# Kernel optimization log

Measured on AMD Instinct MI355X. Metric: run time of the kernel, lower is better.

Reference implementation:

```python
import jax, jax.numpy as jnp
import numpy as np

B, C_IN, T, IMG, P = 4, 3, 8, 224, 16
E, DEPTH, D_INNER, N_ST, DT_R, K = 384, 24, 768, 16, 24, 4
HP = IMG // P
NP_ = HP * HP          # 196 patches per frame
L = T * NP_            # 1568 tokens
EPS = 1e-5


def setup_inputs():
    key = jax.random.key(0)
    ks = jax.random.split(key, 24)
    r = lambda k, s, sc=0.02: jax.random.normal(k, s, jnp.float32) * sc
    inp = {
        "x": jax.random.normal(ks[0], (B, C_IN, T, IMG, IMG), jnp.float32),
        "patch_w": r(ks[1], (E, C_IN, 1, P, P)),
        "patch_b": jnp.zeros((E,), jnp.float32),
        "pos_embed": r(ks[2], (NP_, E)),
        "temporal_pos": r(ks[3], (T, E)),
        "imp_w1": r(ks[4], (E, E)),
        "imp_b1": jnp.zeros((E,), jnp.float32),
        "imp_w2": r(ks[5], (1, E)),
        "imp_b2": jnp.zeros((1,), jnp.float32),
        "in_w": r(ks[6], (DEPTH, 2 * D_INNER, E)),
        "out_w": r(ks[7], (DEPTH, E, D_INNER)),
        "norm_w": jnp.ones((DEPTH, E), jnp.float32),
        "norm_f_w": jnp.ones((E,), jnp.float32),
    }
    A_row = jnp.log(jnp.arange(1, N_ST + 1, dtype=jnp.float32))  # S4D-real init
    for i, sfx in enumerate(["", "_b"]):
        b = 8 + 4 * i
        inp["conv_w" + sfx] = r(ks[b], (DEPTH, D_INNER, K), 0.1)
        inp["conv_b" + sfx] = jnp.zeros((DEPTH, D_INNER), jnp.float32)
        inp["xp_w" + sfx] = r(ks[b + 1], (DEPTH, DT_R + 2 * N_ST, D_INNER))
        inp["dt_w" + sfx] = r(ks[b + 2], (DEPTH, D_INNER, DT_R), 0.01)
        inp["dt_b" + sfx] = jax.random.uniform(ks[b + 3], (DEPTH, D_INNER), jnp.float32, -4.6, -2.3)
        inp["A_log" + sfx] = jnp.tile(A_row, (DEPTH, D_INNER, 1))
        inp["D" + sfx] = jnp.ones((DEPTH, D_INNER), jnp.float32)
    return inp


def rmsnorm(x, w):
    x = x.astype(jnp.float32)
    return x * jax.lax.rsqrt(jnp.mean(x * x, axis=-1, keepdims=True) + EPS) * w


def causal_conv1d(x, w, b):
    # x: [B,L,D]; depthwise causal conv with kernel K
    xt = x.transpose(0, 2, 1)  # B D L
    y = jax.lax.conv_general_dilated(
        xt, w[:, None, :], (1,), [(K - 1, 0)],
        dimension_numbers=("NCH", "OIH", "NCH"), feature_group_count=D_INNER)
    return (y + b[None, :, None]).transpose(0, 2, 1)


def selective_scan(xt, dt, Bm, Cm, A, Dp):
    # xt,dt: [B,L,D]; Bm,Cm: [B,L,N]; A: [D,N]
    def step(h, ins):
        dt_t, x_t, B_t, C_t = ins  # [B,D],[B,D],[B,N],[B,N]
        h = h * jnp.exp(dt_t[..., None] * A) + (dt_t * x_t)[..., None] * B_t[:, None, :]
        return h, jnp.einsum('bdn,bn->bd', h, C_t)
    h0 = jnp.zeros((xt.shape[0], D_INNER, N_ST), xt.dtype)
    xs = (dt.transpose(1, 0, 2), xt.transpose(1, 0, 2),
          Bm.transpose(1, 0, 2), Cm.transpose(1, 0, 2))
    _, ys = jax.lax.scan(step, h0, xs)
    return ys.transpose(1, 0, 2) + xt * Dp


def mamba_dir(xc, z, cw, cb, xpw, dtw, dtb, Alog, Dp):
    xt = jax.nn.silu(causal_conv1d(xc, cw, cb))
    dbc = jnp.einsum('bld,ed->ble', xt, xpw)
    dt_low = dbc[..., :DT_R]
    Bm = dbc[..., DT_R:DT_R + N_ST]
    Cm = dbc[..., DT_R + N_ST:]
    dt = jax.nn.softplus(jnp.einsum('blr,dr->bld', dt_low, dtw) + dtb)
    y = selective_scan(xt, dt, Bm, Cm, -jnp.exp(Alog), Dp)
    return y * jax.nn.silu(z)


def mamba_block(h, p):
    xz = jnp.einsum('ble,fe->blf', h, p['in_w'])
    xc, z = xz[..., :D_INNER], xz[..., D_INNER:]
    yf = mamba_dir(xc, z, p['conv_w'], p['conv_b'], p['xp_w'], p['dt_w'], p['dt_b'], p['A_log'], p['D'])
    flip = lambda t: t[:, ::-1, :]
    yb = flip(mamba_dir(flip(xc), flip(z), p['conv_w_b'], p['conv_b_b'], p['xp_w_b'],
                        p['dt_w_b'], p['dt_b_b'], p['A_log_b'], p['D_b']))
    return jnp.einsum('bld,ed->ble', yf + yb, p['out_w'])


def _encoder(x, patch_w, patch_b, pos_embed, temporal_pos, imp_w1, imp_b1, imp_w2, imp_b2,
             in_w, out_w, norm_w, norm_f_w,
             conv_w, conv_b, xp_w, dt_w, dt_b, A_log, D,
             conv_w_b, conv_b_b, xp_w_b, dt_w_b, dt_b_b, A_log_b, D_b, mixer=mamba_block):
    Bn = x.shape[0]
    # PatchEmbed: Conv3d kernel (1,P,P) stride (1,P,P) == patchify + matmul
    xp = x.reshape(Bn, C_IN, T, HP, P, HP, P)
    xp = xp.transpose(0, 2, 3, 5, 1, 4, 6).reshape(Bn, T, NP_, C_IN * P * P)
    tok = xp @ patch_w.reshape(E, C_IN * P * P).T + patch_b  # [B,T,N,E]
    tok = tok + pos_embed[None, None] + temporal_pos[None, :, None, :]
    xseq = tok.reshape(Bn, L, E)
    # token importance gating
    h1 = jax.nn.relu(xseq @ imp_w1.T + imp_b1)
    logits = (h1 @ imp_w2.T + imp_b2)[..., 0]  # [B,L]
    xseq = xseq * jax.nn.sigmoid(logits)[..., None]
    stacked = {'in_w': in_w, 'out_w': out_w, 'norm_w': norm_w,
               'conv_w': conv_w, 'conv_b': conv_b, 'xp_w': xp_w, 'dt_w': dt_w,
               'dt_b': dt_b, 'A_log': A_log, 'D': D,
               'conv_w_b': conv_w_b, 'conv_b_b': conv_b_b, 'xp_w_b': xp_w_b,
               'dt_w_b': dt_w_b, 'dt_b_b': dt_b_b, 'A_log_b': A_log_b, 'D_b': D_b}

    def layer_fn(carry, p):
        hidden, residual = carry
        residual = (hidden + residual).astype(jnp.float32)  # fused add-norm, prenorm
        hn = rmsnorm(residual, p['norm_w'])
        hidden = mixer(hn, p)
        return (hidden, residual), None

    (hidden, residual), _ = jax.lax.scan(layer_fn, (xseq, jnp.zeros_like(xseq)), stacked)
    feats = rmsnorm(hidden + residual, norm_f_w)
    return feats, logits


def reference(x, patch_w, patch_b, pos_embed, temporal_pos, imp_w1, imp_b1, imp_w2, imp_b2,
              in_w, out_w, norm_w, norm_f_w,
              conv_w, conv_b, xp_w, dt_w, dt_b, A_log, D,
              conv_w_b, conv_b_b, xp_w_b, dt_w_b, dt_b_b, A_log_b, D_b):
    return _encoder(x, patch_w, patch_b, pos_embed, temporal_pos, imp_w1, imp_b1, imp_w2, imp_b2,
                    in_w, out_w, norm_w, norm_f_w,
                    conv_w, conv_b, xp_w, dt_w, dt_b, A_log, D,
                    conv_w_b, conv_b_b, xp_w_b, dt_w_b, dt_b_b, A_log_b, D_b)
```

## Files before the change

### kernel.cpp

```cpp
#include <hip/hip_runtime.h>
#include <hip/hip_bf16.h>

#define LL 1568
#define EE 384
#define DD 768
#define BB 4

typedef float f32x4 __attribute__((ext_vector_type(4)));
typedef float f32x2 __attribute__((ext_vector_type(2)));
typedef unsigned short u16x2 __attribute__((ext_vector_type(2)));
typedef unsigned short u16x4 __attribute__((ext_vector_type(4)));
typedef unsigned short u16x8 __attribute__((ext_vector_type(8)));
typedef __bf16 bf16x8 __attribute__((ext_vector_type(8)));

__device__ inline unsigned short f2bf(float f) {
    unsigned int u = __builtin_bit_cast(unsigned int, f);
    u += 0x7fffu + ((u >> 16) & 1u);
    return (unsigned short)(u >> 16);
}
__device__ inline float bf2f(unsigned short u) {
    unsigned int v = ((unsigned int)u) << 16;
    return __builtin_bit_cast(float, v);
}
__device__ inline float silu_f(float v) { return v / (1.f + __expf(-v)); }
__device__ inline float exp2_f(float v) { return __builtin_amdgcn_exp2f(v); }

__global__ __launch_bounds__(256) void k_cvt(const float* __restrict__ src,
                                             unsigned short* __restrict__ dst, int n4) {
    int i = blockIdx.x * 256 + threadIdx.x;
    int stride = gridDim.x * 256;
    for (; i < n4; i += stride) {
        f32x4 v = *(const f32x4*)(src + (size_t)i * 4);
        u16x4 o;
#pragma unroll
        for (int j = 0; j < 4; j++) o[j] = f2bf(v[j]);
        *(u16x4*)(dst + (size_t)i * 4) = o;
    }
}

__global__ __launch_bounds__(256) void k_pad_xpw(const float* __restrict__ src,
                                                 unsigned short* __restrict__ dst) {
    const int total = 24 * 64 * 768;
    for (int i = blockIdx.x * 256 + threadIdx.x; i < total; i += gridDim.x * 256) {
        int l = i / (64 * 768);
        int r = (i / 768) % 64;
        int dcol = i % 768;
        dst[i] = (r < 56) ? f2bf(src[((size_t)l * 56 + r) * 768 + dcol]) : (unsigned short)0;
    }
}

__global__ __launch_bounds__(256) void k_pad_dtw(const float* __restrict__ src,
                                                 unsigned short* __restrict__ dst) {
    const int total = 24 * 768 * 32;
    for (int i = blockIdx.x * 256 + threadIdx.x; i < total; i += gridDim.x * 256) {
        int kk = i & 31;
        int nrow = i >> 5;
        dst[i] = (kk < 24) ? f2bf(src[(size_t)nrow * 24 + kk]) : (unsigned short)0;
    }
}

__global__ __launch_bounds__(256) void k_patch(const float* __restrict__ x,
                                               unsigned short* __restrict__ patches) {
    int bid = blockIdx.x;
    int b = bid / LL, rr = bid % LL, t = rr / 196, pp = rr % 196, hp = pp / 14, wp = pp % 14;
    for (int k = threadIdx.x; k < 768; k += 256) {
        int c = k >> 8, rem = k & 255, i = rem >> 4, j = rem & 15;
        patches[(size_t)bid * 768 + k] =
            f2bf(x[(((size_t)(b * 3 + c) * 8 + t) * 224 + hp * 16 + i) * 224 + wp * 16 + j]);
    }
}

template <int EPI, bool ASUM, bool OUTBF>
__global__ __launch_bounds__(256) void k_gemm(
    const unsigned short* __restrict__ A, const unsigned short* __restrict__ A2,
    const unsigned short* __restrict__ W,
    float* __restrict__ C, unsigned short* __restrict__ Cb, int K, int ldc,
    const float* __restrict__ bias,
    const float* __restrict__ pos, const float* __restrict__ tpos) {
    const int tid = threadIdx.x;
    const int m0 = blockIdx.y * 128;
    const int n0 = blockIdx.x * 128;
    __shared__ unsigned short As[128 * 40];
    __shared__ unsigned short Ws[128 * 40];
    const int sr = tid >> 2;
    const int skc = tid & 3;

    f32x4 acc[4][4];
#pragma unroll
    for (int mi = 0; mi < 4; mi++)
#pragma unroll
        for (int ni = 0; ni < 4; ni++) acc[mi][ni] = (f32x4){0.f, 0.f, 0.f, 0.f};

    const int lane = tid & 63;
    const int wv = tid >> 6;
    const int wm = (wv & 1) << 6;
    const int wn = (wv >> 1) << 6;
    const int lr = lane & 15;
    const int kg = lane >> 4;

    u16x8 ar[2], wr_[2];
    auto loadT = [&](int kt) {
#pragma unroll
        for (int i = 0; i < 2; i++) {
            size_t ka = (size_t)(m0 + sr + 64 * i) * K + kt * 32 + skc * 8;
            u16x8 v = *(const u16x8*)(A + ka);
            if constexpr (ASUM) {
                u16x8 v2 = *(const u16x8*)(A2 + ka);
#pragma unroll
                for (int j = 0; j < 8; j++) v[j] = f2bf(bf2f(v[j]) + bf2f(v2[j]));
            }
            ar[i] = v;
            wr_[i] = *(const u16x8*)(W + (size_t)(n0 + sr + 64 * i) * K + kt * 32 + skc * 8);
        }
    };

    const int nK = K >> 5;
    loadT(0);
    for (int kt = 0; kt < nK; ++kt) {
#pragma unroll
        for (int i = 0; i < 2; i++) {
            *(u16x8*)&As[(sr + 64 * i) * 40 + skc * 8] = ar[i];
            *(u16x8*)&Ws[(sr + 64 * i) * 40 + skc * 8] = wr_[i];
        }
        __syncthreads();
        if (kt + 1 < nK) loadT(kt + 1);
        bf16x8 af[4], bfm[4];
#pragma unroll
        for (int mi = 0; mi < 4; mi++)
            af[mi] = *(const bf16x8*)&As[(wm + mi * 16 + lr) * 40 + kg * 8];
#pragma unroll
        for (int ni = 0; ni < 4; ni++)
            bfm[ni] = *(const bf16x8*)&Ws[(wn + ni * 16 + lr) * 40 + kg * 8];
#pragma unroll
        for (int mi = 0; mi < 4; mi++)
#pragma unroll
            for (int ni = 0; ni < 4; ni++)
                acc[mi][ni] = __builtin_amdgcn_mfma_f32_16x16x32_bf16(af[mi], bfm[ni], acc[mi][ni], 0, 0, 0);
        __syncthreads();
    }

#pragma unroll
    for (int mi = 0; mi < 4; mi++)
#pragma unroll
        for (int ni = 0; ni < 4; ni++)
#pragma unroll
            for (int j = 0; j < 4; j++) {
                int m = m0 + wm + mi * 16 + kg * 4 + j;
                int n = n0 + wn + ni * 16 + lr;
                float v = acc[mi][ni][j];
                if constexpr (EPI == 1) {
                    int rr = m % LL;
                    int t = rr / 196, p = rr % 196;
                    v += bias[n] + pos[p * EE + n] + tpos[t * EE + n];
                    C[(size_t)m * ldc + n] = v;
                    Cb[(size_t)m * ldc + n] = f2bf(v);
                } else if constexpr (EPI == 2) {
                    v += bias[n];
                    v = fmaxf(v, 0.f);
                    C[(size_t)m * ldc + n] = v;
                } else {
                    if constexpr (OUTBF)
                        Cb[(size_t)m * ldc + n] = f2bf(v);
                    else
                        C[(size_t)m * ldc + n] = v;
                }
            }
}

__global__ __launch_bounds__(64) void k_logits(const float* __restrict__ h1, const float* __restrict__ w2,
                                               const float* __restrict__ b2, float* __restrict__ xseq,
                                               float* __restrict__ logits_out) {
    int row = blockIdx.x;
    int lane = threadIdx.x;
    float acc = 0.f;
#pragma unroll
    for (int i = 0; i < 6; i++) {
        int e = lane + i * 64;
        acc += h1[(size_t)row * EE + e] * w2[e];
    }
#pragma unroll
    for (int off = 32; off >= 1; off >>= 1) acc += __shfl_xor(acc, off);
    float logit = acc + b2[0];
    if (lane == 0) logits_out[row] = logit;
    float sg = 1.f / (1.f + __expf(-logit));
#pragma unroll
    for (int i = 0; i < 6; i++) {
        int e = lane + i * 64;
        xseq[(size_t)row * EE + e] *= sg;
    }
}

template <bool OBF>
__global__ __launch_bounds__(256) void k_norm(const float* __restrict__ hidden, float* __restrict__ resid,
                                              const float* __restrict__ wn, float* __restrict__ outf,
                                              unsigned short* __restrict__ outb,
                                              int first, int writeResid) {
    int row = blockIdx.x * 4 + (threadIdx.x >> 6);
    int lane = threadIdx.x & 63;
    size_t base = (size_t)row * EE;
    float v[6];
    float ss = 0.f;
#pragma unroll
    for (int i = 0; i < 6; i++) {
        int e = lane + i * 64;
        float h = hidden[base + e];
        float r = first ? 0.f : resid[base + e];
        float s = h + r;
        v[i] = s;
        ss += s * s;
    }
#pragma unroll
    for (int off = 32; off >= 1; off >>= 1) ss += __shfl_xor(ss, off);
    if (writeResid) {
#pragma unroll
        for (int i = 0; i < 6; i++) resid[base + lane + i * 64] = v[i];
    }
    float sc = rsqrtf(ss * (1.f / 384.f) + 1e-5f);
#pragma unroll
    for (int i = 0; i < 6; i++) {
        int e = lane + i * 64;
        float o = v[i] * sc * wn[e];
        if constexpr (OBF)
            outb[base + e] = f2bf(o);
        else
            outf[base + e] = o;
    }
}

__global__ __launch_bounds__(256) void k_conv(
    const unsigned short* __restrict__ xz,
    const float* __restrict__ cw_f, const float* __restrict__ cb_f,
    const float* __restrict__ cw_b, const float* __restrict__ cb_b,
    unsigned short* __restrict__ xtb) {
    const int tid = threadIdx.x;
    if (tid >= 192) return;
    const int b = blockIdx.y, dir = blockIdx.z;
    const float* cw = dir ? cw_b : cw_f;
    const float* cb = dir ? cb_b : cb_f;
    const int o = tid % 96, tg = tid / 96;
    const int t0 = blockIdx.x * 16 + tg * 8;
    const int d0 = o * 8;
    const size_t xzb = (size_t)b * LL * 1536;
    const size_t obase = ((size_t)dir * BB + b) * LL;

    f32x4 wq[8];
    float bv[8];
#pragma unroll
    for (int j = 0; j < 8; j++) {
        wq[j] = *(const f32x4*)&cw[(d0 + j) * 4];
        bv[j] = cb[d0 + j];
    }

    auto loadrow = [&](int t) -> u16x8 {
        if (t < 0) return (u16x8){0, 0, 0, 0, 0, 0, 0, 0};
        int phys = dir ? (LL - 1 - t) : t;
        return *(const u16x8*)&xz[xzb + (size_t)phys * 1536 + d0];
    };

    float f0[8], f1[8], f2[8];
    u16x8 v;
    v = loadrow(t0 - 3);
#pragma unroll
    for (int j = 0; j < 8; j++) f0[j] = bf2f(v[j]);
    v = loadrow(t0 - 2);
#pragma unroll
    for (int j = 0; j < 8; j++) f1[j] = bf2f(v[j]);
    v = loadrow(t0 - 1);
#pragma unroll
    for (int j = 0; j < 8; j++) f2[j] = bf2f(v[j]);

    for (int s = 0; s < 8; ++s) {
        int t = t0 + s;
        v = loadrow(t);
        float f3[8];
        u16x8 outv;
#pragma unroll
        for (int j = 0; j < 8; j++) {
            f3[j] = bf2f(v[j]);
            float cv = wq[j][0] * f0[j] + wq[j][1] * f1[j] + wq[j][2] * f2[j] + wq[j][3] * f3[j] + bv[j];
            outv[j] = f2bf(silu_f(cv));
        }
        *(u16x8*)&xtb[(obase + t) * 768 + d0] = outv;
#pragma unroll
        for (int j = 0; j < 8; j++) { f0[j] = f1[j]; f1[j] = f2[j]; f2[j] = f3[j]; }
    }
}

__global__ __launch_bounds__(256) void k_dbc(
    const unsigned short* __restrict__ xtb,
    const unsigned short* __restrict__ xpwb_f, const unsigned short* __restrict__ xpwb_b,
    const unsigned short* __restrict__ dtwb_f, const unsigned short* __restrict__ dtwb_b,
    const float* __restrict__ dtb_f, const float* __restrict__ dtb_b,
    unsigned short* __restrict__ g_dt, float* __restrict__ Bm, float* __restrict__ Cm) {
    const int tid = threadIdx.x;
    const int m0 = blockIdx.x * 64;
    const bool bwd = (m0 >= 6272);
    const unsigned short* W = bwd ? xpwb_b : xpwb_f;
    __shared__ unsigned short As[64 * 40];
    __shared__ unsigned short Ws[64 * 40];
    __shared__ unsigned short Ds[64 * 40];
    const int sr = tid >> 2, skc = tid & 3;
    const int lane = tid & 63, wv = tid >> 6;
    const int lr = lane & 15, kg = lane >> 4;

    f32x4 acc[4];
#pragma unroll
    for (int mi = 0; mi < 4; mi++) acc[mi] = (f32x4){0.f, 0.f, 0.f, 0.f};

    u16x8 ar, wr_;
    auto loadT = [&](int kt) {
        ar = *(const u16x8*)(xtb + (size_t)(m0 + sr) * 768 + kt * 32 + skc * 8);
        wr_ = *(const u16x8*)(W + (size_t)sr * 768 + kt * 32 + skc * 8);
    };
    loadT(0);
    for (int kt = 0; kt < 24; ++kt) {
        *(u16x8*)&As[sr * 40 + skc * 8] = ar;
        *(u16x8*)&Ws[sr * 40 + skc * 8] = wr_;
        __syncthreads();
        if (kt + 1 < 24) loadT(kt + 1);
        bf16x8 bfm = *(const bf16x8*)&Ws[(wv * 16 + lr) * 40 + kg * 8];
#pragma unroll
        for (int mi = 0; mi < 4; mi++) {
            bf16x8 af = *(const bf16x8*)&As[(mi * 16 + lr) * 40 + kg * 8];
            acc[mi] = __builtin_amdgcn_mfma_f32_16x16x32_bf16(af, bfm, acc[mi], 0, 0, 0);
        }
        __syncthreads();
    }
#pragma unroll
    for (int mi = 0; mi < 4; mi++)
#pragma unroll
        for (int j = 0; j < 4; j++) {
            int r = mi * 16 + kg * 4 + j;
            int row = m0 + r;
            int cc = wv * 16 + lr;
            float vv = acc[mi][j];
            if (cc < 32) Ds[r * 40 + cc] = (cc < 24) ? f2bf(vv) : (unsigned short)0;
            if (cc >= 24 && cc < 40) Bm[(size_t)row * 16 + (cc - 24)] = vv;
            else if (cc >= 40 && cc < 56) Cm[(size_t)row * 16 + (cc - 40)] = vv;
        }
    __syncthreads();

    const unsigned short* dtw = bwd ? dtwb_b : dtwb_f;
    const float* dbias = bwd ? dtb_b : dtb_f;
    bf16x8 af2[4];
#pragma unroll
    for (int mi = 0; mi < 4; mi++)
        af2[mi] = *(const bf16x8*)&Ds[(mi * 16 + lr) * 40 + kg * 8];
    for (int nt = wv; nt < 12; nt += 4) {
        int n0 = nt * 64;
        f32x4 acc2[4][4];
#pragma unroll
        for (int mi = 0; mi < 4; mi++)
#pragma unroll
            for (int ni = 0; ni < 4; ni++) acc2[mi][ni] = (f32x4){0.f, 0.f, 0.f, 0.f};
        bf16x8 bfr[4];
#pragma unroll
        for (int ni = 0; ni < 4; ni++)
            bfr[ni] = *(const bf16x8*)(dtw + (size_t)(n0 + ni * 16 + lr) * 32 + kg * 8);
#pragma unroll
        for (int mi = 0; mi < 4; mi++)
#pragma unroll
            for (int ni = 0; ni < 4; ni++)
                acc2[mi][ni] = __builtin_amdgcn_mfma_f32_16x16x32_bf16(af2[mi], bfr[ni], acc2[mi][ni], 0, 0, 0);
#pragma unroll
        for (int mi = 0; mi < 4; mi++)
#pragma unroll
            for (int ni = 0; ni < 4; ni++)
#pragma unroll
                for (int j = 0; j < 4; j++) {
                    int r = mi * 16 + kg * 4 + j;
                    int n = n0 + ni * 16 + lr;
                    float v = acc2[mi][ni][j] + dbias[n];
                    float sp = (v > 20.f) ? v : log1pf(__expf(v));
                    g_dt[(size_t)(m0 + r) * 768 + n] = f2bf(sp);
                }
    }
}

__global__ __launch_bounds__(512) void k_scan(
    const unsigned short* __restrict__ xtb, const unsigned short* __restrict__ dtb,
    const unsigned short* __restrict__ xz,
    const float* __restrict__ Bmat, const float* __restrict__ Cmat,
    const float* __restrict__ Alog_f, const float* __restrict__ Alog_b,
    const float* __restrict__ Dp_f, const float* __restrict__ Dp_b,
    unsigned short* __restrict__ ybuf) {
    const int tid = threadIdx.x;
    const int dl = tid & 15, c = tid >> 4;
    const int d0 = blockIdx.x * 32 + dl * 2;
    const int b = blockIdx.y, dir = blockIdx.z;
    const float* Alog = dir ? Alog_b : Alog_f;
    const float* Dp = dir ? Dp_b : Dp_f;
    const int t0 = c * 49;

    __shared__ float Ssh[32][32][17];
    __shared__ float sdt_sh[32][32];

    float anA[16], anB[16];
#pragma unroll
    for (int n = 0; n < 16; n++) {
        anA[n] = -__expf(Alog[d0 * 16 + n]) * 1.44269504f;
        anB[n] = -__expf(Alog[(d0 + 1) * 16 + n]) * 1.44269504f;
    }
    bool unif = (anA[0] != 0.f) && (anB[0] != 0.f);
#pragma unroll
    for (int n = 1; n < 16; n++) {
        float rA = anA[n] / anA[0];
        float rB = anB[n] / anB[0];
        unif = unif && (fabsf(rA - (float)(n + 1)) < 1e-3f) && (fabsf(rB - (float)(n + 1)) < 1e-3f);
    }
    const float a0A = anA[0], a0B = anB[0];
    float DdA = Dp[d0], DdB = Dp[d0 + 1];

    const size_t dbase = ((size_t)dir * BB + b) * LL;
    const size_t rowb = dbase * 768 + d0;

    f32x2 SA[8], SB[8];
#pragma unroll
    for (int k = 0; k < 8; k++) { SA[k] = (f32x2){0.f, 0.f}; SB[k] = (f32x2){0.f, 0.f}; }
    float sumA = 0.f, sumB = 0.f;

    for (int s = 0; s < 49; ++s) {
        int t = t0 + s;
        unsigned int xv = *(const unsigned int*)&xtb[rowb + (size_t)t * 768];
        unsigned int dv = *(const unsigned int*)&dtb[rowb + (size_t)t * 768];
        float xtA = bf2f((unsigned short)xv), xtB = bf2f((unsigned short)(xv >> 16));
        float dtA = bf2f((unsigned short)dv), dtB = bf2f((unsigned short)(dv >> 16));
        sumA += dtA; sumB += dtB;
        float dxA = dtA * xtA, dxB = dtB * xtB;
        const f32x4* Bp = (const f32x4*)(Bmat + (dbase + t) * 16);
        f32x4 Bq[4] = {Bp[0], Bp[1], Bp[2], Bp[3]};
        const f32x2* B2 = (const f32x2*)Bq;
        f32x2 dxA2 = {dxA, dxA}, dxB2 = {dxB, dxB};
        if (unif) {
            float pA = exp2_f(dtA * a0A), pB = exp2_f(dtB * a0B);
            float qA = pA * pA, qB = pB * pB;
            f32x2 qA2 = {qA, qA}, qB2 = {qB, qB};
            f32x2 pwA[8], pwB[8];
            pwA[0] = (f32x2){pA, qA};
            pwB[0] = (f32x2){pB, qB};
#pragma unroll
            for (int j = 1; j < 8; j++) { pwA[j] = pwA[j - 1] * qA2; pwB[j] = pwB[j - 1] * qB2; }
#pragma unroll
            for (int k = 0; k < 8; k++) {
                SA[k] = SA[k] * pwA[k] + dxA2 * B2[k];
                SB[k] = SB[k] * pwB[k] + dxB2 * B2[k];
            }
        } else {
#pragma unroll
            for (int n = 0; n < 16; n++) {
                float bqv = ((const float*)Bq)[n];
                float eA = exp2_f(dtA * anA[n]);
                float eB = exp2_f(dtB * anB[n]);
                SA[n >> 1][n & 1] = SA[n >> 1][n & 1] * eA + dxA * bqv;
                SB[n >> 1][n & 1] = SB[n >> 1][n & 1] * eB + dxB * bqv;
            }
        }
    }
#pragma unroll
    for (int n = 0; n < 16; n++) {
        Ssh[c][dl * 2][n] = SA[n >> 1][n & 1];
        Ssh[c][dl * 2 + 1][n] = SB[n >> 1][n & 1];
    }
    sdt_sh[c][dl * 2] = sumA;
    sdt_sh[c][dl * 2 + 1] = sumB;
    __syncthreads();

    {
        int cdl = tid & 31, n2 = tid >> 5;
        float a_n = -__expf(Alog[(blockIdx.x * 32 + cdl) * 16 + n2]) * 1.44269504f;
        float H = 0.f;
#pragma unroll
        for (int c2 = 0; c2 < 32; c2++) {
            float P = exp2_f(a_n * sdt_sh[c2][cdl]);
            float tmp = Ssh[c2][cdl][n2];
            Ssh[c2][cdl][n2] = H;
            H = H * P + tmp;
        }
    }
    __syncthreads();

#pragma unroll
    for (int n = 0; n < 16; n++) {
        SA[n >> 1][n & 1] = Ssh[c][dl * 2][n];
        SB[n >> 1][n & 1] = Ssh[c][dl * 2 + 1][n];
    }
    for (int s = 0; s < 49; ++s) {
        int t = t0 + s;
        unsigned int xv = *(const unsigned int*)&xtb[rowb + (size_t)t * 768];
        unsigned int dv = *(const unsigned int*)&dtb[rowb + (size_t)t * 768];
        float xtA = bf2f((unsigned short)xv), xtB = bf2f((unsigned short)(xv >> 16));
        float dtA = bf2f((unsigned short)dv), dtB = bf2f((unsigned short)(dv >> 16));
        float dxA = dtA * xtA, dxB = dtB * xtB;
        const f32x4* Bp = (const f32x4*)(Bmat + (dbase + t) * 16);
        f32x4 Bq[4] = {Bp[0], Bp[1], Bp[2], Bp[3]};
        const f32x4* Cp = (const f32x4*)(Cmat + (dbase + t) * 16);
        f32x4 Cq[4] = {Cp[0], Cp[1], Cp[2], Cp[3]};
        const f32x2* B2 = (const f32x2*)Bq;
        const f32x2* C2 = (const f32x2*)Cq;
        f32x2 dxA2 = {dxA, dxA}, dxB2 = {dxB, dxB};
        f32x2 yA2 = {0.f, 0.f}, yB2 = {0.f, 0.f};
        if (unif) {
            float pA = exp2_f(dtA * a0A), pB = exp2_f(dtB * a0B);
            float qA = pA * pA, qB = pB * pB;
            f32x2 qA2 = {qA, qA}, qB2 = {qB, qB};
            f32x2 pwA[8], pwB[8];
            pwA[0] = (f32x2){pA, qA};
            pwB[0] = (f32x2){pB, qB};
#pragma unroll
            for (int j = 1; j < 8; j++) { pwA[j] = pwA[j - 1] * qA2; pwB[j] = pwB[j - 1] * qB2; }
#pragma unroll
            for (int k = 0; k < 8; k++) {
                SA[k] = SA[k] * pwA[k] + dxA2 * B2[k];
                SB[k] = SB[k] * pwB[k] + dxB2 * B2[k];
                yA2 = yA2 + SA[k] * C2[k];
                yB2 = yB2 + SB[k] * C2[k];
            }
        } else {
#pragma unroll
            for (int n = 0; n < 16; n++) {
                float bqv = ((const float*)Bq)[n];
                float cqv = ((const float*)Cq)[n];
                float eA = exp2_f(dtA * anA[n]);
                float eB = exp2_f(dtB * anB[n]);
                float sA = SA[n >> 1][n & 1] * eA + dxA * bqv;
                float sB = SB[n >> 1][n & 1] * eB + dxB * bqv;
                SA[n >> 1][n & 1] = sA;
                SB[n >> 1][n & 1] = sB;
                yA2[n & 1] += sA * cqv;
                yB2[n & 1] += sB * cqv;
            }
        }
        float yA = yA2[0] + yA2[1] + xtA * DdA;
        float yB = yB2[0] + yB2[1] + xtB * DdB;
        int pt = dir ? (LL - 1 - t) : t;
        unsigned int zv2 = *(const unsigned int*)&xz[((size_t)b * LL + pt) * 1536 + 768 + d0];
        float zA = bf2f((unsigned short)zv2), zB = bf2f((unsigned short)(zv2 >> 16));
        unsigned int yo = (unsigned int)f2bf(yA * silu_f(zA)) |
                          ((unsigned int)f2bf(yB * silu_f(zB)) << 16);
        *(unsigned int*)&ybuf[rowb + (size_t)pt * 768] = yo;
    }
}

extern "C" void kernel_launch(void* const* d_in, const int* in_sizes, int n_in,
                              void* d_out, int out_size, void* d_ws, size_t ws_size,
                              hipStream_t stream) {
    const float* x        = (const float*)d_in[0];
    const float* patch_w  = (const float*)d_in[1];
    const float* patch_b  = (const float*)d_in[2];
    const float* pos_emb  = (const float*)d_in[3];
    const float* tpos     = (const float*)d_in[4];
    const float* imp_w1   = (const float*)d_in[5];
    const float* imp_b1   = (const float*)d_in[6];
    const float* imp_w2   = (const float*)d_in[7];
    const float* imp_b2   = (const float*)d_in[8];
    const float* in_w     = (const float*)d_in[9];
    const float* out_w    = (const float*)d_in[10];
    const float* norm_w   = (const float*)d_in[11];
    const float* norm_f_w = (const float*)d_in[12];
    const float* conv_w   = (const float*)d_in[13];
    const float* conv_b   = (const float*)d_in[14];
    const float* xp_w     = (const float*)d_in[15];
    const float* dt_w     = (const float*)d_in[16];
    const float* dt_b     = (const float*)d_in[17];
    const float* A_log    = (const float*)d_in[18];
    const float* Dp       = (const float*)d_in[19];
    const float* conv_w_b = (const float*)d_in[20];
    const float* conv_b_b = (const float*)d_in[21];
    const float* xp_w_b   = (const float*)d_in[22];
    const float* dt_w_b   = (const float*)d_in[23];
    const float* dt_b_b   = (const float*)d_in[24];
    const float* A_log_b  = (const float*)d_in[25];
    const float* D_b      = (const float*)d_in[26];

    float* out = (float*)d_out;
    float* logits_out = out + 2408448;

    char* wsb = (char*)d_ws;
    size_t off = 0;
    auto carve = [&](size_t bytes) { char* p = wsb + off; off += bytes; return p; };

    unsigned short* in_wb    = (unsigned short*)carve(28311552);
    unsigned short* out_wb   = (unsigned short*)carve(14155776);
    unsigned short* patch_wb = (unsigned short*)carve(589824);
    unsigned short* imp_w1b  = (unsigned short*)carve(294912);
    unsigned short* xpwb_f   = (unsigned short*)carve(2359296);
    unsigned short* xpwb_b   = (unsigned short*)carve(2359296);
    unsigned short* dtwb_f   = (unsigned short*)carve(1179648);
    unsigned short* dtwb_b   = (unsigned short*)carve(1179648);
    float*          hidden   = (float*)carve(9633792);
    float*          resid    = (float*)carve(9633792);
    unsigned short* hn       = (unsigned short*)carve(4816896);
    unsigned short* xzb      = (unsigned short*)carve(19267584);
    unsigned short* xtb      = (unsigned short*)carve(19267584);
    unsigned short* g_dt     = (unsigned short*)carve(19267584);
    float*          Bm       = (float*)carve(802816);
    float*          Cm       = (float*)carve(802816);
    unsigned short* ybuf     = (unsigned short*)carve(19267584);

    float*          h1       = (float*)xtb;
    unsigned short* hidb     = (unsigned short*)g_dt;
    unsigned short* patches  = (unsigned short*)ybuf;

    k_cvt<<<2048, 256, 0, stream>>>(in_w, in_wb, 3538944);
    k_cvt<<<2048, 256, 0, stream>>>(out_w, out_wb, 1769472);
    k_cvt<<<288, 256, 0, stream>>>(patch_w, patch_wb, 73728);
    k_cvt<<<144, 256, 0, stream>>>(imp_w1, imp_w1b, 36864);
    k_pad_xpw<<<1024, 256, 0, stream>>>(xp_w, xpwb_f);
    k_pad_xpw<<<1024, 256, 0, stream>>>(xp_w_b, xpwb_b);
    k_pad_dtw<<<1024, 256, 0, stream>>>(dt_w, dtwb_f);
    k_pad_dtw<<<1024, 256, 0, stream>>>(dt_w_b, dtwb_b);

    k_patch<<<6272, 256, 0, stream>>>(x, patches);
    k_gemm<1, false, false><<<dim3(3, 49), 256, 0, stream>>>(patches, nullptr, patch_wb,
                                                             hidden, hidb, 768, 384,
                                                             patch_b, pos_emb, tpos);
    k_gemm<2, false, false><<<dim3(3, 49), 256, 0, stream>>>(hidb, nullptr, imp_w1b,
                                                             h1, nullptr, 384, 384,
                                                             imp_b1, nullptr, nullptr);
    k_logits<<<6272, 64, 0, stream>>>(h1, imp_w2, imp_b2, hidden, logits_out);

    for (int l = 0; l < 24; ++l) {
        k_norm<true><<<1568, 256, 0, stream>>>(hidden, resid, norm_w + l * 384, nullptr, hn,
                                               (l == 0) ? 1 : 0, 1);
        k_gemm<0, false, true><<<dim3(12, 49), 256, 0, stream>>>(hn, nullptr,
                                                                 in_wb + (size_t)l * 589824,
                                                                 nullptr, xzb, 384, 1536,
                                                                 nullptr, nullptr, nullptr);
        k_conv<<<dim3(98, 4, 2), 256, 0, stream>>>(xzb, conv_w + l * 3072, conv_b + l * 768,
                                                   conv_w_b + l * 3072, conv_b_b + l * 768, xtb);
        k_dbc<<<196, 256, 0, stream>>>(xtb, xpwb_f + (size_t)l * 49152, xpwb_b + (size_t)l * 49152,
                                       dtwb_f + (size_t)l * 24576, dtwb_b + (size_t)l * 24576,
                                       dt_b + l * 768, dt_b_b + l * 768,
                                       g_dt, Bm, Cm);
        k_scan<<<dim3(24, 4, 2), 512, 0, stream>>>(
            xtb, g_dt, xzb, Bm, Cm,
            A_log + l * 12288, A_log_b + l * 12288,
            Dp + l * 768, D_b + l * 768,
            ybuf);
        k_gemm<0, true, false><<<dim3(3, 49), 256, 0, stream>>>(ybuf, ybuf + 4816896,
                                                                out_wb + (size_t)l * 294912,
                                                                hidden, nullptr, 768, 384,
                                                                nullptr, nullptr, nullptr);
    }
    k_norm<false><<<1568, 256, 0, stream>>>(hidden, resid, norm_f_w, out, nullptr, 0, 0);
}
```

Baseline: 5.280 ms.

## Split dt projection out of k_dbc into a separate tiled GEMM launch

The fused k_dbc kernel previously did both the x-projection and the dt up-projection (K=32 to 768 with softplus) inside only 196 blocks. The change has k_dbc write a padded 32-wide low-rank dt buffer to global memory, then launches the generic GEMM with a new softplus epilogue over a 6x98 grid. The epilogue picks forward or backward weights and bias by row. This spreads the dt GEMM and the expensive softplus across many more blocks, at the cost of an extra launch and a small global round-trip per layer.

```diff
diff --git a/kernel.cpp b/kernel.cpp
--- a/kernel.cpp
+++ b/kernel.cpp
@@ -73,9 +73,9 @@
 template <int EPI, bool ASUM, bool OUTBF>
 __global__ __launch_bounds__(256) void k_gemm(
     const unsigned short* __restrict__ A, const unsigned short* __restrict__ A2,
-    const unsigned short* __restrict__ W,
+    const unsigned short* __restrict__ W, const unsigned short* __restrict__ W2,
     float* __restrict__ C, unsigned short* __restrict__ Cb, int K, int ldc,
-    const float* __restrict__ bias,
+    const float* __restrict__ bias, const float* __restrict__ bias2,
     const float* __restrict__ pos, const float* __restrict__ tpos) {
     const int tid = threadIdx.x;
     const int m0 = blockIdx.y * 128;
@@ -85,6 +85,12 @@
     const int sr = tid >> 2;
     const int skc = tid & 3;
 
+    const unsigned short* Wp = W;
+    const float* biasp = bias;
+    if constexpr (EPI == 3) {
+        if (m0 >= 6272) { Wp = W2; biasp = bias2; }
+    }
+
     f32x4 acc[4][4];
 #pragma unroll
     for (int mi = 0; mi < 4; mi++)
@@ -110,7 +116,7 @@
                 for (int j = 0; j < 8; j++) v[j] = f2bf(bf2f(v[j]) + bf2f(v2[j]));
             }
             ar[i] = v;
-            wr_[i] = *(const u16x8*)(W + (size_t)(n0 + sr + 64 * i) * K + kt * 32 + skc * 8);
+            wr_[i] = *(const u16x8*)(Wp + (size_t)(n0 + sr + 64 * i) * K + kt * 32 + skc * 8);
         }
     };
 
@@ -158,6 +164,10 @@
                     v += bias[n];
                     v = fmaxf(v, 0.f);
                     C[(size_t)m * ldc + n] = v;
+                } else if constexpr (EPI == 3) {
+                    v += biasp[n];
+                    float sp = (v > 20.f) ? v : log1pf(__expf(v));
+                    Cb[(size_t)m * ldc + n] = f2bf(sp);
                 } else {
                     if constexpr (OUTBF)
                         Cb[(size_t)m * ldc + n] = f2bf(v);
@@ -289,16 +299,12 @@
 __global__ __launch_bounds__(256) void k_dbc(
     const unsigned short* __restrict__ xtb,
     const unsigned short* __restrict__ xpwb_f, const unsigned short* __restrict__ xpwb_b,
-    const unsigned short* __restrict__ dtwb_f, const unsigned short* __restrict__ dtwb_b,
-    const float* __restrict__ dtb_f, const float* __restrict__ dtb_b,
-    unsigned short* __restrict__ g_dt, float* __restrict__ Bm, float* __restrict__ Cm) {
+    unsigned short* __restrict__ dtlow, float* __restrict__ Bm, float* __restrict__ Cm) {
     const int tid = threadIdx.x;
     const int m0 = blockIdx.x * 64;
-    const bool bwd = (m0 >= 6272);
-    const unsigned short* W = bwd ? xpwb_b : xpwb_f;
+    const unsigned short* W = (m0 >= 6272) ? xpwb_b : xpwb_f;
     __shared__ unsigned short As[64 * 40];
     __shared__ unsigned short Ws[64 * 40];
-    __shared__ unsigned short Ds[64 * 40];
     const int sr = tid >> 2, skc = tid & 3;
     const int lane = tid & 63, wv = tid >> 6;
     const int lr = lane & 15, kg = lane >> 4;
@@ -330,51 +336,14 @@
     for (int mi = 0; mi < 4; mi++)
 #pragma unroll
         for (int j = 0; j < 4; j++) {
-            int r = mi * 16 + kg * 4 + j;
-            int row = m0 + r;
+            int row = m0 + mi * 16 + kg * 4 + j;
             int cc = wv * 16 + lr;
             float vv = acc[mi][j];
-            if (cc < 32) Ds[r * 40 + cc] = (cc < 24) ? f2bf(vv) : (unsigned short)0;
-            if (cc >= 24 && cc < 40) Bm[(size_t)row * 16 + (cc - 24)] = vv;
-            else if (cc >= 40 && cc < 56) Cm[(size_t)row * 16 + (cc - 40)] = vv;
-        }
-    __syncthreads();
-
-    const unsigned short* dtw = bwd ? dtwb_b : dtwb_f;
-    const float* dbias = bwd ? dtb_b : dtb_f;
-    bf16x8 af2[4];
-#pragma unroll
-    for (int mi = 0; mi < 4; mi++)
-        af2[mi] = *(const bf16x8*)&Ds[(mi * 16 + lr) * 40 + kg * 8];
-    for (int nt = wv; nt < 12; nt += 4) {
-        int n0 = nt * 64;
-        f32x4 acc2[4][4];
-#pragma unroll
-        for (int mi = 0; mi < 4; mi++)
-#pragma unroll
-            for (int ni = 0; ni < 4; ni++) acc2[mi][ni] = (f32x4){0.f, 0.f, 0.f, 0.f};
-        bf16x8 bfr[4];
-#pragma unroll
-        for (int ni = 0; ni < 4; ni++)
-            bfr[ni] = *(const bf16x8*)(dtw + (size_t)(n0 + ni * 16 + lr) * 32 + kg * 8);
-#pragma unroll
-        for (int mi = 0; mi < 4; mi++)
-#pragma unroll
-            for (int ni = 0; ni < 4; ni++)
-                acc2[mi][ni] = __builtin_amdgcn_mfma_f32_16x16x32_bf16(af2[mi], bfr[ni], acc2[mi][ni], 0, 0, 0);
-#pragma unroll
-        for (int mi = 0; mi < 4; mi++)
-#pragma unroll
-            for (int ni = 0; ni < 4; ni++)
-#pragma unroll
-                for (int j = 0; j < 4; j++) {
-                    int r = mi * 16 + kg * 4 + j;
-                    int n = n0 + ni * 16 + lr;
-                    float v = acc2[mi][ni][j] + dbias[n];
-                    float sp = (v > 20.f) ? v : log1pf(__expf(v));
-                    g_dt[(size_t)(m0 + r) * 768 + n] = f2bf(sp);
-                }
-    }
+            if (cc < 24) dtlow[(size_t)row * 32 + cc] = f2bf(vv);
+            else if (cc < 40) Bm[(size_t)row * 16 + (cc - 24)] = vv;
+            else if (cc < 56) Cm[(size_t)row * 16 + (cc - 40)] = vv;
+            else dtlow[(size_t)row * 32 + (cc - 32)] = 0;
+        }
 }
 
 __global__ __launch_bounds__(512) void k_scan(
@@ -593,6 +562,7 @@
     unsigned short* xzb      = (unsigned short*)carve(19267584);
     unsigned short* xtb      = (unsigned short*)carve(19267584);
     unsigned short* g_dt     = (unsigned short*)carve(19267584);
+    unsigned short* dtlow    = (unsigned short*)carve(802816);
     float*          Bm       = (float*)carve(802816);
     float*          Cm       = (float*)carve(802816);
     unsigned short* ybuf     = (unsigned short*)carve(19267584);
@@ -611,36 +581,39 @@
     k_pad_dtw<<<1024, 256, 0, stream>>>(dt_w_b, dtwb_b);
 
     k_patch<<<6272, 256, 0, stream>>>(x, patches);
-    k_gemm<1, false, false><<<dim3(3, 49), 256, 0, stream>>>(patches, nullptr, patch_wb,
+    k_gemm<1, false, false><<<dim3(3, 49), 256, 0, stream>>>(patches, nullptr, patch_wb, nullptr,
                                                              hidden, hidb, 768, 384,
-                                                             patch_b, pos_emb, tpos);
-    k_gemm<2, false, false><<<dim3(3, 49), 256, 0, stream>>>(hidb, nullptr, imp_w1b,
+                                                             patch_b, nullptr, pos_emb, tpos);
+    k_gemm<2, false, false><<<dim3(3, 49), 256, 0, stream>>>(hidb, nullptr, imp_w1b, nullptr,
                                                              h1, nullptr, 384, 384,
-                                                             imp_b1, nullptr, nullptr);
+                                                             imp_b1, nullptr, nullptr, nullptr);
     k_logits<<<6272, 64, 0, stream>>>(h1, imp_w2, imp_b2, hidden, logits_out);
 
     for (int l = 0; l < 24; ++l) {
         k_norm<true><<<1568, 256, 0, stream>>>(hidden, resid, norm_w + l * 384, nullptr, hn,
                                                (l == 0) ? 1 : 0, 1);
-        k_gemm<0, false, true><<<dim3(12, 49), 256, 0, stream>>>(hn, nullptr,
-                                                                 in_wb + (size_t)l * 589824,
-                                                                 nullptr, xzb, 384, 1536,
-                                                                 nullptr, nullptr, nullptr);
+        k_gemm<0, false, true><<<dim3(12, 49), 256, 0, stream>>>(hn, nullptr, in_wb + (size_t)l * 589824,
+                                                                 nullptr, nullptr, xzb, 384, 1536,
+                                                                 nullptr, nullptr, nullptr, nullptr);
         k_conv<<<dim3(98, 4, 2), 256, 0, stream>>>(xzb, conv_w + l * 3072, conv_b + l * 768,
                                                    conv_w_b + l * 3072, conv_b_b + l * 768, xtb);
         k_dbc<<<196, 256, 0, stream>>>(xtb, xpwb_f + (size_t)l * 49152, xpwb_b + (size_t)l * 49152,
-                                       dtwb_f + (size_t)l * 24576, dtwb_b + (size_t)l * 24576,
-                                       dt_b + l * 768, dt_b_b + l * 768,
-                                       g_dt, Bm, Cm);
+                                       dtlow, Bm, Cm);
+        k_gemm<3, false, true><<<dim3(6, 98), 256, 0, stream>>>(dtlow, nullptr,
+                                                                dtwb_f + (size_t)l * 24576,
+                                                                dtwb_b + (size_t)l * 24576,
+                                                                nullptr, g_dt, 32, 768,
+                                                                dt_b + l * 768, dt_b_b + l * 768,
+                                                                nullptr, nullptr);
         k_scan<<<dim3(24, 4, 2), 512, 0, stream>>>(
             xtb, g_dt, xzb, Bm, Cm,
             A_log + l * 12288, A_log_b + l * 12288,
             Dp + l * 768, D_b + l * 768,
             ybuf);
         k_gemm<0, true, false><<<dim3(3, 49), 256, 0, stream>>>(ybuf, ybuf + 4816896,
-                                                                out_wb + (size_t)l * 294912,
+                                                                out_wb + (size_t)l * 294912, nullptr,
                                                                 hidden, nullptr, 768, 384,
-                                                                nullptr, nullptr, nullptr);
+                                                                nullptr, nullptr, nullptr, nullptr);
     }
     k_norm<false><<<1568, 256, 0, stream>>>(hidden, resid, norm_f_w, out, nullptr, 0, 0);
 }
```

Result: faster. 5.033 ms (-4.7%).
